# Kernel optimization log

Measured on AMD Instinct MI355X. Metric: run time of the kernel, lower is better.

Reference implementation:

```python
import jax, jax.numpy as jnp
import numpy as np

# Graph geometry: G complete graphs (molecules) of n nodes each.
N_PER_G, G, DEG = 64, 256, 16
H, D = 8, 8
IN_DIM = H * D      # 64
EDGE_DIM = 64
N = N_PER_G * G                      # 16384 nodes
EF = G * N_PER_G * N_PER_G           # 1,048,576 full edges
ES = G * N_PER_G * DEG               # 262,144 sparse edges
SCALE = float(np.sqrt(D))


def _edges():
    n = N_PER_G
    # full graph: all (i -> j) pairs per block, edge id = b*n*n + i*n + j
    ij = np.arange(n * n)
    i, j = ij // n, ij % n
    b = np.arange(G)[:, None]
    src_full = (b * n + i[None, :]).reshape(-1).astype(np.int32)
    dst_full = (b * n + j[None, :]).reshape(-1).astype(np.int32)
    # sparse graph: each dst j receives from DEG distinct sources (j+1..j+DEG mod n)
    jj = np.arange(n)[:, None]
    kk = np.arange(DEG)[None, :]
    ii = (jj + 1 + kk) % n
    eid_block = (ii * n + jj).reshape(-1)                 # [n*DEG]
    sparse_eid = (np.arange(G)[:, None] * n * n + eid_block[None, :]).reshape(-1).astype(np.int32)
    return jnp.asarray(src_full), jnp.asarray(dst_full), jnp.asarray(sparse_eid)


def setup_inputs() -> dict:
    key = jax.random.key(0)
    ks = jax.random.split(key, 16)
    w = lambda k, shape, s=0.05: s * jax.random.normal(k, shape, jnp.float32)
    src_full, dst_full, sparse_eid = _edges()
    return dict(
        h=jax.random.normal(ks[0], (N, IN_DIM), jnp.float32),
        e=jax.random.normal(ks[1], (ES, EDGE_DIM), jnp.float32),
        adj2=jax.random.uniform(ks[2], (EF,), jnp.float32),
        rel_pos_3d=jax.random.normal(ks[3], (EF, H), jnp.float32),
        Wq=w(ks[4], (H * D, IN_DIM)), bq=jnp.zeros((H * D,), jnp.float32),
        Wk=w(ks[5], (H * D, IN_DIM)), bk=jnp.zeros((H * D,), jnp.float32),
        Wv=w(ks[6], (H * D, IN_DIM)), bv=jnp.zeros((H * D,), jnp.float32),
        Wpe=w(ks[7], (H, EDGE_DIM)), bpe=jnp.zeros((H,), jnp.float32),
        Wap=w(ks[8], (EDGE_DIM, H)), bap=jnp.zeros((EDGE_DIM,), jnp.float32),
        Wo=w(ks[9], (H * D, H * D)), bo=jnp.zeros((H * D,), jnp.float32),
        Woe=w(ks[10], (EDGE_DIM, EDGE_DIM)), boe=jnp.zeros((EDGE_DIM,), jnp.float32),
        src_full=src_full, dst_full=dst_full, sparse_eid=sparse_eid,
    )


def reference(h, e, adj2, rel_pos_3d, Wq, bq, Wk, bk, Wv, bv, Wpe, bpe,
              Wap, bap, Wo, bo, Woe, boe, src_full, dst_full, sparse_eid):
    Qh = (h @ Wq.T + bq).reshape(N, H, D)
    Kh = (h @ Wk.T + bk).reshape(N, H, D)
    Vh = (h @ Wv.T + bv).reshape(N, H, D)
    proj_e = e @ Wpe.T + bpe                                   # [ES, H]
    # edge-wise QK dot (src=K, dst=Q), scaled, then gaussian-decay + rel-pos bias
    score = jnp.sum(Kh[src_full] * Qh[dst_full], axis=-1) / SCALE   # [EF, H]
    score = score * adj2[:, None] + rel_pos_3d                      # [EF, H]
    # gather sparse-subgraph scores, project for edge output, add proj_e bias
    sc_sp = score[sparse_eid]                                        # [ES, H]
    e_out_raw = sc_sp @ Wap.T + bap                                  # [ES, EDGE_DIM]
    score = score.at[sparse_eid].set(sc_sp + proj_e)
    # edge softmax over incoming edges of each destination node
    logits = jnp.clip(score, -5.0, 5.0)
    m = jax.ops.segment_max(logits, dst_full, num_segments=N)
    ex = jnp.exp(logits - m[dst_full])
    den = jax.ops.segment_sum(ex, dst_full, num_segments=N)
    attn = ex / den[dst_full]                                        # [EF, H]
    # weighted scatter-sum of source values
    wV = jax.ops.segment_sum(Vh[src_full] * attn[..., None], dst_full, num_segments=N)
    h_out = wV.reshape(N, H * D) @ Wo.T + bo
    e_out = (e_out_raw + e) @ Woe.T + boe
    return h_out, e_out
```

## Files before the change

kernel.cpp:

```cpp
#include <hip/hip_runtime.h>


__global__ __launch_bounds__(512, 2) void qkvpe_kernel(
    const float* __restrict__ h,
    const float* __restrict__ e,
    const float* __restrict__ Wq, const float* __restrict__ bq,
    const float* __restrict__ Wk, const float* __restrict__ bk,
    const float* __restrict__ Wv, const float* __restrict__ bv,
    const float* __restrict__ Wpe, const float* __restrict__ bpe,
    float* __restrict__ Qs, float* __restrict__ Ks, float* __restrict__ Vs,
    float* __restrict__ PEs)
{
    const int t = threadIdx.x;
    if (blockIdx.x < 256) {
        const int b    = blockIdx.x;
        const int lane = t & 63;
        const int wu   = __builtin_amdgcn_readfirstlane(t >> 6);
        const float* hrow = h + (size_t)(b * 64 + lane) * 64;
        float accQ[8], accK[8], accV[8];
        #pragma unroll
        for (int cc = 0; cc < 8; ++cc) {
            const int c = wu * 8 + cc;
            accQ[cc] = bq[c]; accK[cc] = bk[c]; accV[cc] = bv[c];
        }
        #pragma unroll 1
        for (int k0 = 0; k0 < 4; ++k0) {
            float hv[16];
            #pragma unroll
            for (int u = 0; u < 4; ++u) {
                const float4 x = ((const float4*)hrow)[k0 * 4 + u];
                hv[u*4+0] = x.x; hv[u*4+1] = x.y; hv[u*4+2] = x.z; hv[u*4+3] = x.w;
            }
            #pragma unroll
            for (int cc = 0; cc < 8; ++cc) {
                const int c = wu * 8 + cc;
                const float* wq  = Wq + c * 64 + k0 * 16;
                const float* wk  = Wk + c * 64 + k0 * 16;
                const float* wvp = Wv + c * 64 + k0 * 16;
                #pragma unroll
                for (int k = 0; k < 16; ++k) {
                    accQ[cc] = fmaf(hv[k], wq[k],  accQ[cc]);
                    accK[cc] = fmaf(hv[k], wk[k],  accK[cc]);
                    accV[cc] = fmaf(hv[k], wvp[k], accV[cc]);
                }
            }
        }
        const size_t o = (size_t)(b * 64 + lane) * 64 + wu * 8;
        *(float4*)(Qs + o)     = make_float4(accQ[0], accQ[1], accQ[2], accQ[3]);
        *(float4*)(Qs + o + 4) = make_float4(accQ[4], accQ[5], accQ[6], accQ[7]);
        *(float4*)(Ks + o)     = make_float4(accK[0], accK[1], accK[2], accK[3]);
        *(float4*)(Ks + o + 4) = make_float4(accK[4], accK[5], accK[6], accK[7]);
        *(float4*)(Vs + o)     = make_float4(accV[0], accV[1], accV[2], accV[3]);
        *(float4*)(Vs + o + 4) = make_float4(accV[4], accV[5], accV[6], accV[7]);
    } else {
        const int row = (blockIdx.x - 256) * 512 + t;
        const float* erow = e + (size_t)row * 64;
        float acc[8];
        #pragma unroll
        for (int h2 = 0; h2 < 8; ++h2) acc[h2] = bpe[h2];
        #pragma unroll 1
        for (int k0 = 0; k0 < 4; ++k0) {
            float ev[16];
            #pragma unroll
            for (int u = 0; u < 4; ++u) {
                const float4 x = ((const float4*)erow)[k0 * 4 + u];
                ev[u*4+0] = x.x; ev[u*4+1] = x.y; ev[u*4+2] = x.z; ev[u*4+3] = x.w;
            }
            #pragma unroll
            for (int h2 = 0; h2 < 8; ++h2) {
                const float* wp = Wpe + h2 * 64 + k0 * 16;
                #pragma unroll
                for (int k = 0; k < 16; ++k)
                    acc[h2] = fmaf(ev[k], wp[k], acc[h2]);
            }
        }
        float* p0 = PEs + (size_t)row * 8;
        *(float4*)(p0)     = make_float4(acc[0], acc[1], acc[2], acc[3]);
        *(float4*)(p0 + 4) = make_float4(acc[4], acc[5], acc[6], acc[7]);
    }
}

__global__ __launch_bounds__(256, 2) void attn_kernel(
    const float* __restrict__ Qs, const float* __restrict__ Ks,
    const float* __restrict__ Vs, const float* __restrict__ PEs,
    const float* __restrict__ adj2,
    const float* __restrict__ rel,
    float* __restrict__ wVg,
    float* __restrict__ scsp)
{
    const int b2   = blockIdx.x;
    const int b    = b2 >> 1;
    const int joff = (b2 & 1) << 5;
    const int t    = threadIdx.x;
    const int j    = joff + (t >> 3);
    const int hh   = t & 7;

    const float* kB   = Ks + (size_t)b * 4096 + hh * 8;
    const float* vB   = Vs + (size_t)b * 4096 + hh * 8;
    const float* relP = rel + ((size_t)b * 4096 + j) * 8 + hh;
    const float* adjP = adj2 + (size_t)b * 4096 + j;
    const float* peP  = PEs + ((size_t)b * 1024 + j * 16) * 8 + hh;

    float q[8];
    {
        const float* qp = Qs + (size_t)(b * 64 + j) * 64 + hh * 8;
        const float4 a = *(const float4*)qp;
        const float4 c = *(const float4*)(qp + 4);
        q[0]=a.x; q[1]=a.y; q[2]=a.z; q[3]=a.w;
        q[4]=c.x; q[5]=c.y; q[6]=c.z; q[7]=c.w;
    }

    float den = 0.f;
    float wv[8] = {0.f,0.f,0.f,0.f,0.f,0.f,0.f,0.f};
    float sc[16];
    const float inv_scale = 0.35355339059327379f;

    #pragma unroll
    for (int m = 0; m < 16; ++m) {
        const int i = (j + 1 + m) & 63;
        const float4 kA = *(const float4*)(kB + i * 64);
        const float4 kBv = *(const float4*)(kB + i * 64 + 4);
        const float rp = relP[(size_t)i * 512];
        const float a2 = adjP[(size_t)i * 64];
        const float pe = peP[m * 8];
        float s = kA.x * q[0];
        s = fmaf(kA.y, q[1], s); s = fmaf(kA.z, q[2], s); s = fmaf(kA.w, q[3], s);
        s = fmaf(kBv.x, q[4], s); s = fmaf(kBv.y, q[5], s); s = fmaf(kBv.z, q[6], s);
        s = fmaf(kBv.w, q[7], s);
        s = fmaf(s * inv_scale, a2, rp);
        sc[m] = s;
        s += pe;
        s = fminf(fmaxf(s, -5.f), 5.f);
        const float ex = __expf(s);
        den += ex;
        const float4 vA = *(const float4*)(vB + i * 64);
        const float4 vBv = *(const float4*)(vB + i * 64 + 4);
        wv[0] = fmaf(ex, vA.x, wv[0]); wv[1] = fmaf(ex, vA.y, wv[1]);
        wv[2] = fmaf(ex, vA.z, wv[2]); wv[3] = fmaf(ex, vA.w, wv[3]);
        wv[4] = fmaf(ex, vBv.x, wv[4]); wv[5] = fmaf(ex, vBv.y, wv[5]);
        wv[6] = fmaf(ex, vBv.z, wv[6]); wv[7] = fmaf(ex, vBv.w, wv[7]);
    }
    #pragma unroll 8
    for (int m = 16; m < 64; ++m) {
        const int i = (j + 1 + m) & 63;
        const float4 kA = *(const float4*)(kB + i * 64);
        const float4 kBv = *(const float4*)(kB + i * 64 + 4);
        const float rp = relP[(size_t)i * 512];
        const float a2 = adjP[(size_t)i * 64];
        float s = kA.x * q[0];
        s = fmaf(kA.y, q[1], s); s = fmaf(kA.z, q[2], s); s = fmaf(kA.w, q[3], s);
        s = fmaf(kBv.x, q[4], s); s = fmaf(kBv.y, q[5], s); s = fmaf(kBv.z, q[6], s);
        s = fmaf(kBv.w, q[7], s);
        s = fmaf(s * inv_scale, a2, rp);
        s = fminf(fmaxf(s, -5.f), 5.f);
        const float ex = __expf(s);
        den += ex;
        const float4 vA = *(const float4*)(vB + i * 64);
        const float4 vBv = *(const float4*)(vB + i * 64 + 4);
        wv[0] = fmaf(ex, vA.x, wv[0]); wv[1] = fmaf(ex, vA.y, wv[1]);
        wv[2] = fmaf(ex, vA.z, wv[2]); wv[3] = fmaf(ex, vA.w, wv[3]);
        wv[4] = fmaf(ex, vBv.x, wv[4]); wv[5] = fmaf(ex, vBv.y, wv[5]);
        wv[6] = fmaf(ex, vBv.z, wv[6]); wv[7] = fmaf(ex, vBv.w, wv[7]);
    }

    float* sp = scsp + ((size_t)b * 1024 + j * 16) * 8 + hh;
    #pragma unroll
    for (int m = 0; m < 16; ++m) sp[m * 8] = sc[m];

    const float id = 1.f / den;
    float* wp = wVg + (size_t)(b * 64 + j) * 64 + hh * 8;
    *(float4*)(wp)     = make_float4(wv[0]*id, wv[1]*id, wv[2]*id, wv[3]*id);
    *(float4*)(wp + 4) = make_float4(wv[4]*id, wv[5]*id, wv[6]*id, wv[7]*id);
}

__global__ __launch_bounds__(256, 2) void hout_kernel(
    const float* __restrict__ wVg,
    const float* __restrict__ Wo, const float* __restrict__ bo,
    float* __restrict__ h_out)
{
    __shared__ float shWT[64 * 69];
    __shared__ float shWoT[64 * 65];

    const int t    = threadIdx.x;
    const int base = blockIdx.x * 64;

    {
        const int r0 = t >> 2, qq = t & 3;
        const float* ep = wVg + (size_t)(base + r0) * 64 + qq * 16;
        #pragma unroll
        for (int v = 0; v < 4; ++v) {
            const float4 x = ((const float4*)ep)[v];
            const int c = qq * 16 + v * 4;
            shWT[(c + 0) * 69 + r0] = x.x;
            shWT[(c + 1) * 69 + r0] = x.y;
            shWT[(c + 2) * 69 + r0] = x.z;
            shWT[(c + 3) * 69 + r0] = x.w;
        }
    }
    {
        const int c0 = t >> 2, qq = t & 3;
        const float* wp = Wo + c0 * 64 + qq * 16;
        #pragma unroll
        for (int v = 0; v < 4; ++v) {
            const float4 x = ((const float4*)wp)[v];
            const int k = qq * 16 + v * 4;
            shWoT[(k + 0) * 65 + c0] = x.x;
            shWoT[(k + 1) * 65 + c0] = x.y;
            shWoT[(k + 2) * 65 + c0] = x.z;
            shWoT[(k + 3) * 65 + c0] = x.w;
        }
    }
    __syncthreads();

    const int rq = t >> 4;
    const int cq = t & 15;
    float acc[16];
    {
        const float4 bv = *(const float4*)(bo + cq * 4);
        #pragma unroll
        for (int ri = 0; ri < 4; ++ri) {
            acc[ri*4+0] = bv.x; acc[ri*4+1] = bv.y;
            acc[ri*4+2] = bv.z; acc[ri*4+3] = bv.w;
        }
    }
    #pragma unroll
    for (int k = 0; k < 64; ++k) {
        const float4 ev = *(const float4*)&shWT[k * 69 + rq * 4];
        const float4 wk = *(const float4*)&shWoT[k * 65 + cq * 4];
        acc[0]  = fmaf(ev.x, wk.x, acc[0]);  acc[1]  = fmaf(ev.x, wk.y, acc[1]);
        acc[2]  = fmaf(ev.x, wk.z, acc[2]);  acc[3]  = fmaf(ev.x, wk.w, acc[3]);
        acc[4]  = fmaf(ev.y, wk.x, acc[4]);  acc[5]  = fmaf(ev.y, wk.y, acc[5]);
        acc[6]  = fmaf(ev.y, wk.z, acc[6]);  acc[7]  = fmaf(ev.y, wk.w, acc[7]);
        acc[8]  = fmaf(ev.z, wk.x, acc[8]);  acc[9]  = fmaf(ev.z, wk.y, acc[9]);
        acc[10] = fmaf(ev.z, wk.z, acc[10]); acc[11] = fmaf(ev.z, wk.w, acc[11]);
        acc[12] = fmaf(ev.w, wk.x, acc[12]); acc[13] = fmaf(ev.w, wk.y, acc[13]);
        acc[14] = fmaf(ev.w, wk.z, acc[14]); acc[15] = fmaf(ev.w, wk.w, acc[15]);
    }
    #pragma unroll
    for (int ri = 0; ri < 4; ++ri) {
        float* orow = h_out + (size_t)(base + rq * 4 + ri) * 64 + cq * 4;
        *(float4*)orow = make_float4(acc[ri*4+0], acc[ri*4+1], acc[ri*4+2], acc[ri*4+3]);
    }
}

__global__ void prep_kernel(const float* __restrict__ Wap, const float* __restrict__ bap,
                            const float* __restrict__ Woe, const float* __restrict__ boe,
                            float* __restrict__ M2, float* __restrict__ Tm, int hasT)
{
    const int tg = blockIdx.x * 64 + threadIdx.x;
    if (tg < 512) {
        const int c = tg >> 3, hq = tg & 7;
        float s = 0.f;
        #pragma unroll 8
        for (int k = 0; k < 64; ++k) s = fmaf(Woe[c * 64 + k], Wap[k * 8 + hq], s);
        M2[tg] = s;
    } else if (tg < 576) {
        const int c = tg - 512;
        float s = boe[c];
        #pragma unroll 8
        for (int k = 0; k < 64; ++k) s = fmaf(bap[k], Woe[c * 64 + k], s);
        M2[512 + c] = s;
    } else if (hasT && tg < 576 + 73 * 64) {
        const int idx = tg - 576;
        const int k = idx >> 6, c = idx & 63;
        float v;
        if (k < 64) {
            v = Woe[c * 64 + k];
        } else if (k < 72) {
            const int hq = k - 64;
            v = 0.f;
            #pragma unroll 8
            for (int kk = 0; kk < 64; ++kk)
                v = fmaf(Woe[c * 64 + kk], Wap[kk * 8 + hq], v);
        } else {
            v = boe[c];
            #pragma unroll 8
            for (int kk = 0; kk < 64; ++kk)
                v = fmaf(bap[kk], Woe[c * 64 + kk], v);
        }
        Tm[k * 64 + c] = v;
    }
}

__global__ __launch_bounds__(256, 2) void eoutT_kernel(
    const float* __restrict__ e,
    const float* __restrict__ scsp,
    const float* __restrict__ Tm,
    float* __restrict__ e_out)
{
    __shared__ float shET[72 * 69];
    __shared__ float shTm[73 * 64];

    const int t    = threadIdx.x;
    const int base = blockIdx.x * 64;

    {
        const int r0 = t >> 2, qq = t & 3;
        const float* ep = e + (size_t)(base + r0) * 64 + qq * 16;
        #pragma unroll
        for (int v = 0; v < 4; ++v) {
            const float4 x = ((const float4*)ep)[v];
            const int c = qq * 16 + v * 4;
            shET[(c + 0) * 69 + r0] = x.x;
            shET[(c + 1) * 69 + r0] = x.y;
            shET[(c + 2) * 69 + r0] = x.z;
            shET[(c + 3) * 69 + r0] = x.w;
        }
    }
    if (t < 128) {
        const int r = t >> 1, pp = t & 1;
        const float4 s4 = *(const float4*)(scsp + (size_t)(base + r) * 8 + pp * 4);
        shET[(64 + pp * 4 + 0) * 69 + r] = s4.x;
        shET[(64 + pp * 4 + 1) * 69 + r] = s4.y;
        shET[(64 + pp * 4 + 2) * 69 + r] = s4.z;
        shET[(64 + pp * 4 + 3) * 69 + r] = s4.w;
    }
    #pragma unroll
    for (int v = 0; v < 5; ++v) {
        const int fi = v * 256 + t;
        if (fi < 1168)
            *(float4*)&shTm[fi * 4] = *(const float4*)(Tm + fi * 4);
    }
    __syncthreads();

    const int rq = t >> 4;
    const int cq = t & 15;
    float acc[16];
    {
        const float4 bcv = *(const float4*)&shTm[72 * 64 + cq * 4];
        #pragma unroll
        for (int ri = 0; ri < 4; ++ri) {
            acc[ri*4+0] = bcv.x; acc[ri*4+1] = bcv.y;
            acc[ri*4+2] = bcv.z; acc[ri*4+3] = bcv.w;
        }
    }
    #pragma unroll
    for (int k = 0; k < 72; ++k) {
        const float4 ev = *(const float4*)&shET[k * 69 + rq * 4];
        const float4 wk = *(const float4*)&shTm[k * 64 + cq * 4];
        acc[0]  = fmaf(ev.x, wk.x, acc[0]);  acc[1]  = fmaf(ev.x, wk.y, acc[1]);
        acc[2]  = fmaf(ev.x, wk.z, acc[2]);  acc[3]  = fmaf(ev.x, wk.w, acc[3]);
        acc[4]  = fmaf(ev.y, wk.x, acc[4]);  acc[5]  = fmaf(ev.y, wk.y, acc[5]);
        acc[6]  = fmaf(ev.y, wk.z, acc[6]);  acc[7]  = fmaf(ev.y, wk.w, acc[7]);
        acc[8]  = fmaf(ev.z, wk.x, acc[8]);  acc[9]  = fmaf(ev.z, wk.y, acc[9]);
        acc[10] = fmaf(ev.z, wk.z, acc[10]); acc[11] = fmaf(ev.z, wk.w, acc[11]);
        acc[12] = fmaf(ev.w, wk.x, acc[12]); acc[13] = fmaf(ev.w, wk.y, acc[13]);
        acc[14] = fmaf(ev.w, wk.z, acc[14]); acc[15] = fmaf(ev.w, wk.w, acc[15]);
    }
    #pragma unroll
    for (int ri = 0; ri < 4; ++ri) {
        float* orow = e_out + (size_t)(base + rq * 4 + ri) * 64 + cq * 4;
        *(float4*)orow = make_float4(acc[ri*4+0], acc[ri*4+1], acc[ri*4+2], acc[ri*4+3]);
    }
}

__global__ __launch_bounds__(256, 2) void eout_kernel(
    const float* __restrict__ e,
    const float* __restrict__ scsp,
    const float* __restrict__ Woe,
    const float* __restrict__ M2g,
    float* __restrict__ e_out)
{
    __shared__ float shE[64 * 64];
    __shared__ float shS[64 * 8];
    const int t    = threadIdx.x;
    const int base = blockIdx.x * 64;
    {
        const int r = t >> 2, qq = t & 3;
        const float* ep = e + (size_t)(base + r) * 64 + qq * 16;
        #pragma unroll
        for (int u = 0; u < 4; ++u) {
            const float4 x = ((const float4*)ep)[u];
            const int cc = qq * 4 + u;
            *(float4*)&shE[r * 64 + ((cc ^ (r & 15)) << 2)] = x;
        }
    }
    if (t < 128) {
        const int r = t >> 1, pp = t & 1;
        *(float4*)&shS[r * 8 + pp * 4] =
            *(const float4*)(scsp + (size_t)(base + r) * 8 + pp * 4);
    }
    __syncthreads();
    const int w = __builtin_amdgcn_readfirstlane(t >> 6);
    const int r = t & 63;
    float sc[8];
    {
        const float4 a  = *(const float4*)&shS[r * 8];
        const float4 c4 = *(const float4*)&shS[r * 8 + 4];
        sc[0]=a.x; sc[1]=a.y; sc[2]=a.z; sc[3]=a.w;
        sc[4]=c4.x; sc[5]=c4.y; sc[6]=c4.z; sc[7]=c4.w;
    }
    float acc[16];
    #pragma unroll
    for (int u = 0; u < 16; ++u) {
        const int c = w * 16 + u;
        float s = M2g[512 + c];
        #pragma unroll
        for (int hq = 0; hq < 8; ++hq)
            s = fmaf(sc[hq], M2g[c * 8 + hq], s);
        acc[u] = s;
    }
    #pragma unroll
    for (int k0 = 0; k0 < 4; ++k0) {
        float ev[16];
        #pragma unroll
        for (int v = 0; v < 4; ++v) {
            const int cc = k0 * 4 + v;
            const float4 x = *(const float4*)&shE[r * 64 + ((cc ^ (r & 15)) << 2)];
            ev[v*4+0] = x.x; ev[v*4+1] = x.y; ev[v*4+2] = x.z; ev[v*4+3] = x.w;
        }
        #pragma unroll
        for (int u = 0; u < 16; ++u) {
            const float* wr = Woe + (w * 16 + u) * 64 + k0 * 16;
            #pragma unroll
            for (int k = 0; k < 16; ++k)
                acc[u] = fmaf(ev[k], wr[k], acc[u]);
        }
    }
    float* orow = e_out + (size_t)(base + r) * 64 + w * 16;
    #pragma unroll
    for (int u = 0; u < 4; ++u)
        *(float4*)&orow[u * 4] =
            make_float4(acc[u*4+0], acc[u*4+1], acc[u*4+2], acc[u*4+3]);
}

extern "C" void kernel_launch(void* const* d_in, const int* in_sizes, int n_in,
                              void* d_out, int out_size, void* d_ws, size_t ws_size,
                              hipStream_t stream) {
    const float* h    = (const float*)d_in[0];
    const float* e    = (const float*)d_in[1];
    const float* adj2 = (const float*)d_in[2];
    const float* rel  = (const float*)d_in[3];
    const float* Wq   = (const float*)d_in[4];  const float* bq  = (const float*)d_in[5];
    const float* Wk   = (const float*)d_in[6];  const float* bk  = (const float*)d_in[7];
    const float* Wv   = (const float*)d_in[8];  const float* bv  = (const float*)d_in[9];
    const float* Wpe  = (const float*)d_in[10]; const float* bpe = (const float*)d_in[11];
    const float* Wap  = (const float*)d_in[12]; const float* bap = (const float*)d_in[13];
    const float* Wo   = (const float*)d_in[14]; const float* bo  = (const float*)d_in[15];
    const float* Woe  = (const float*)d_in[16]; const float* boe = (const float*)d_in[17];

    float* out  = (float*)d_out;
    float* hout = out;
    float* eout = out + 16384 * 64;
    float* Qs   = eout;
    float* Ks   = eout + 1048576;
    float* Vs   = eout + 2097152;
    float* PEs  = eout + 3145728;
    float* ws   = (float*)d_ws;
    float* scsp = ws;
    float* M2g  = ws + 2097152;
    float* Tm   = ws + 2098176;
    const int hasT = (ws_size >= (size_t)(2098176 + 73 * 64) * sizeof(float)) ? 1 : 0;

    prep_kernel<<<dim3(82), dim3(64), 0, stream>>>(Wap, bap, Woe, boe, M2g, Tm, hasT);
    qkvpe_kernel<<<dim3(768), dim3(512), 0, stream>>>(
        h, e, Wq, bq, Wk, bk, Wv, bv, Wpe, bpe, Qs, Ks, Vs, PEs);
    attn_kernel<<<dim3(512), dim3(256), 0, stream>>>(
        Qs, Ks, Vs, PEs, adj2, rel, hout , scsp);
    hout_kernel<<<dim3(256), dim3(256), 0, stream>>>(hout, Wo, bo, hout);
    if (hasT)
        eoutT_kernel<<<dim3(4096), dim3(256), 0, stream>>>(e, scsp, Tm, eout);
    else
        eout_kernel<<<dim3(4096), dim3(256), 0, stream>>>(e, scsp, Woe, M2g, eout);
}
```

Measured before the change: 130.8 us.

## Pre-transpose adj2/rel in prep kernel and stage K/V/PE in LDS for attention

Adds extra blocks to the QKV/PE kernel that transpose adj2 and rel_pos_3d per graph into a layout contiguous per destination node. The attention kernel then loads those rows with float4 into registers and stages K, V and PE for the whole graph in shared memory, using one 512-thread block per graph. Sparse-edge scores are written in place into the shared PE buffer and copied out in one coalesced pass. This replaces strided global reads with contiguous ones, but it adds an extra full read and write of rel and adj2 through global scratch, uses large register arrays (R and A, 64 each), and drops attention occupancy to one block per CU.

```diff
diff --git a/kernel.cpp b/kernel.cpp
--- a/kernel.cpp
+++ b/kernel.cpp
@@ -4,13 +4,17 @@
 __global__ __launch_bounds__(512, 2) void qkvpe_kernel(
     const float* __restrict__ h,
     const float* __restrict__ e,
+    const float* __restrict__ adj2,
+    const float* __restrict__ rel,
     const float* __restrict__ Wq, const float* __restrict__ bq,
     const float* __restrict__ Wk, const float* __restrict__ bk,
     const float* __restrict__ Wv, const float* __restrict__ bv,
     const float* __restrict__ Wpe, const float* __restrict__ bpe,
     float* __restrict__ Qs, float* __restrict__ Ks, float* __restrict__ Vs,
-    float* __restrict__ PEs)
+    float* __restrict__ PEs, float* __restrict__ relT, float* __restrict__ adjT)
 {
+    __shared__ float shA[64 * 65];
+    __shared__ float shR[8 * 576];
     const int t = threadIdx.x;
     if (blockIdx.x < 256) {
         const int b    = blockIdx.x;
@@ -52,7 +56,7 @@
         *(float4*)(Ks + o + 4) = make_float4(accK[4], accK[5], accK[6], accK[7]);
         *(float4*)(Vs + o)     = make_float4(accV[0], accV[1], accV[2], accV[3]);
         *(float4*)(Vs + o + 4) = make_float4(accV[4], accV[5], accV[6], accV[7]);
-    } else {
+    } else if (blockIdx.x < 768) {
         const int row = (blockIdx.x - 256) * 512 + t;
         const float* erow = e + (size_t)row * 64;
         float acc[8];
@@ -77,96 +81,135 @@
         float* p0 = PEs + (size_t)row * 8;
         *(float4*)(p0)     = make_float4(acc[0], acc[1], acc[2], acc[3]);
         *(float4*)(p0 + 4) = make_float4(acc[4], acc[5], acc[6], acc[7]);
-    }
-}
-
-__global__ __launch_bounds__(256, 2) void attn_kernel(
+    } else {
+        const int b = blockIdx.x - 768;
+        {
+            const float* ap = adj2 + (size_t)b * 4096 + t * 8;
+            #pragma unroll
+            for (int d = 0; d < 8; ++d)
+                shA[((t & 7) * 8 + d) * 65 + (t >> 3)] = ap[d];
+        }
+        __syncthreads();
+        {
+            const int jj = t >> 3, io = (t & 7) * 8;
+            float* op = adjT + (size_t)b * 4096 + jj * 64 + io;
+            #pragma unroll
+            for (int d = 0; d < 8; ++d)
+                op[d] = shA[jj * 65 + io + d];
+        }
+        #pragma unroll 1
+        for (int c = 0; c < 8; ++c) {
+            __syncthreads();
+            {
+                const float* rp = rel + (size_t)b * 32768 + c * 4096 + t * 8;
+                const int i8 = t >> 6;
+                const int g  = t & 63;
+                #pragma unroll
+                for (int d = 0; d < 8; ++d)
+                    shR[i8 * 576 + g * 9 + d] = rp[d];
+            }
+            __syncthreads();
+            {
+                float* op = relT + (size_t)b * 32768 + (size_t)t * 64 + c * 8;
+                const int g = t >> 3, d0 = t & 7;
+                #pragma unroll
+                for (int i8 = 0; i8 < 8; ++i8)
+                    op[i8] = shR[i8 * 576 + g * 9 + d0];
+            }
+        }
+    }
+}
+
+__global__ __launch_bounds__(512, 1) void attn_kernel(
     const float* __restrict__ Qs, const float* __restrict__ Ks,
     const float* __restrict__ Vs, const float* __restrict__ PEs,
-    const float* __restrict__ adj2,
-    const float* __restrict__ rel,
+    const float* __restrict__ adjT,
+    const float* __restrict__ relT,
     float* __restrict__ wVg,
     float* __restrict__ scsp)
 {
-    const int b2   = blockIdx.x;
-    const int b    = b2 >> 1;
-    const int joff = (b2 & 1) << 5;
-    const int t    = threadIdx.x;
-    const int j    = joff + (t >> 3);
-    const int hh   = t & 7;
-
-    const float* kB   = Ks + (size_t)b * 4096 + hh * 8;
-    const float* vB   = Vs + (size_t)b * 4096 + hh * 8;
-    const float* relP = rel + ((size_t)b * 4096 + j) * 8 + hh;
-    const float* adjP = adj2 + (size_t)b * 4096 + j;
-    const float* peP  = PEs + ((size_t)b * 1024 + j * 16) * 8 + hh;
-
+    __shared__ float shK[64 * 64];
+    __shared__ float shV[64 * 64];
+    __shared__ float shPE[1024 * 8];
+
+    const int b  = blockIdx.x;
+    const int t  = threadIdx.x;
+    const int j  = t >> 3;
+    const int hh = t & 7;
+
+    const float* rT = relT + (size_t)b * 32768 + (size_t)t * 64;
+    const float* aT = adjT + (size_t)b * 4096 + (size_t)j * 64;
+    float R[64], A[64];
+    #pragma unroll
+    for (int u = 0; u < 16; ++u) {
+        const float4 x = *(const float4*)(rT + u * 4);
+        R[u*4+0] = x.x; R[u*4+1] = x.y; R[u*4+2] = x.z; R[u*4+3] = x.w;
+        const float4 y = *(const float4*)(aT + u * 4);
+        A[u*4+0] = y.x; A[u*4+1] = y.y; A[u*4+2] = y.z; A[u*4+3] = y.w;
+    }
+    {
+        const float4* srcK = (const float4*)(Ks + (size_t)b * 4096);
+        const float4* srcV = (const float4*)(Vs + (size_t)b * 4096);
+        float4* dK = (float4*)shK; float4* dV = (float4*)shV;
+        #pragma unroll
+        for (int u = 0; u < 2; ++u) {
+            dK[u * 512 + t] = srcK[u * 512 + t];
+            dV[u * 512 + t] = srcV[u * 512 + t];
+        }
+        const float4* srcP = (const float4*)(PEs + (size_t)b * 8192);
+        float4* dP = (float4*)shPE;
+        #pragma unroll
+        for (int u = 0; u < 4; ++u)
+            dP[u * 512 + t] = srcP[u * 512 + t];
+    }
     float q[8];
     {
         const float* qp = Qs + (size_t)(b * 64 + j) * 64 + hh * 8;
         const float4 a = *(const float4*)qp;
-        const float4 c = *(const float4*)(qp + 4);
+        const float4 c4 = *(const float4*)(qp + 4);
         q[0]=a.x; q[1]=a.y; q[2]=a.z; q[3]=a.w;
-        q[4]=c.x; q[5]=c.y; q[6]=c.z; q[7]=c.w;
-    }
+        q[4]=c4.x; q[5]=c4.y; q[6]=c4.z; q[7]=c4.w;
+    }
+    __syncthreads();
 
     float den = 0.f;
     float wv[8] = {0.f,0.f,0.f,0.f,0.f,0.f,0.f,0.f};
-    float sc[16];
     const float inv_scale = 0.35355339059327379f;
-
-    #pragma unroll
-    for (int m = 0; m < 16; ++m) {
-        const int i = (j + 1 + m) & 63;
-        const float4 kA = *(const float4*)(kB + i * 64);
-        const float4 kBv = *(const float4*)(kB + i * 64 + 4);
-        const float rp = relP[(size_t)i * 512];
-        const float a2 = adjP[(size_t)i * 64];
-        const float pe = peP[m * 8];
+    #pragma unroll
+    for (int i = 0; i < 64; ++i) {
+        const float4 kA = *(const float4*)&shK[i * 64 + hh * 8];
+        const float4 kC = *(const float4*)&shK[i * 64 + hh * 8 + 4];
         float s = kA.x * q[0];
         s = fmaf(kA.y, q[1], s); s = fmaf(kA.z, q[2], s); s = fmaf(kA.w, q[3], s);
-        s = fmaf(kBv.x, q[4], s); s = fmaf(kBv.y, q[5], s); s = fmaf(kBv.z, q[6], s);
-        s = fmaf(kBv.w, q[7], s);
-        s = fmaf(s * inv_scale, a2, rp);
-        sc[m] = s;
-        s += pe;
+        s = fmaf(kC.x, q[4], s); s = fmaf(kC.y, q[5], s); s = fmaf(kC.z, q[6], s);
+        s = fmaf(kC.w, q[7], s);
+        s = fmaf(s * inv_scale, A[i], R[i]);
+        const int kidx = (i - j - 1) & 63;
+        if (kidx < 16) {
+            const int x = (j * 16 + kidx) * 8 + hh;
+            const float pe = shPE[x];
+            shPE[x] = s;
+            s += pe;
+        }
         s = fminf(fmaxf(s, -5.f), 5.f);
         const float ex = __expf(s);
         den += ex;
-        const float4 vA = *(const float4*)(vB + i * 64);
-        const float4 vBv = *(const float4*)(vB + i * 64 + 4);
+        const float4 vA = *(const float4*)&shV[i * 64 + hh * 8];
+        const float4 vC = *(const float4*)&shV[i * 64 + hh * 8 + 4];
         wv[0] = fmaf(ex, vA.x, wv[0]); wv[1] = fmaf(ex, vA.y, wv[1]);
         wv[2] = fmaf(ex, vA.z, wv[2]); wv[3] = fmaf(ex, vA.w, wv[3]);
-        wv[4] = fmaf(ex, vBv.x, wv[4]); wv[5] = fmaf(ex, vBv.y, wv[5]);
-        wv[6] = fmaf(ex, vBv.z, wv[6]); wv[7] = fmaf(ex, vBv.w, wv[7]);
-    }
-    #pragma unroll 8
-    for (int m = 16; m < 64; ++m) {
-        const int i = (j + 1 + m) & 63;
-        const float4 kA = *(const float4*)(kB + i * 64);
-        const float4 kBv = *(const float4*)(kB + i * 64 + 4);
-        const float rp = relP[(size_t)i * 512];
-        const float a2 = adjP[(size_t)i * 64];
-        float s = kA.x * q[0];
-        s = fmaf(kA.y, q[1], s); s = fmaf(kA.z, q[2], s); s = fmaf(kA.w, q[3], s);
-        s = fmaf(kBv.x, q[4], s); s = fmaf(kBv.y, q[5], s); s = fmaf(kBv.z, q[6], s);
-        s = fmaf(kBv.w, q[7], s);
-        s = fmaf(s * inv_scale, a2, rp);
-        s = fminf(fmaxf(s, -5.f), 5.f);
-        const float ex = __expf(s);
-        den += ex;
-        const float4 vA = *(const float4*)(vB + i * 64);
-        const float4 vBv = *(const float4*)(vB + i * 64 + 4);
-        wv[0] = fmaf(ex, vA.x, wv[0]); wv[1] = fmaf(ex, vA.y, wv[1]);
-        wv[2] = fmaf(ex, vA.z, wv[2]); wv[3] = fmaf(ex, vA.w, wv[3]);
-        wv[4] = fmaf(ex, vBv.x, wv[4]); wv[5] = fmaf(ex, vBv.y, wv[5]);
-        wv[6] = fmaf(ex, vBv.z, wv[6]); wv[7] = fmaf(ex, vBv.w, wv[7]);
-    }
-
-    float* sp = scsp + ((size_t)b * 1024 + j * 16) * 8 + hh;
-    #pragma unroll
-    for (int m = 0; m < 16; ++m) sp[m * 8] = sc[m];
-
+        wv[4] = fmaf(ex, vC.x, wv[4]); wv[5] = fmaf(ex, vC.y, wv[5]);
+        wv[6] = fmaf(ex, vC.z, wv[6]); wv[7] = fmaf(ex, vC.w, wv[7]);
+    }
+    __syncthreads();
+
+    {
+        const float4* src = (const float4*)shPE;
+        float4* dst = (float4*)(scsp + (size_t)b * 8192);
+        #pragma unroll
+        for (int u = 0; u < 4; ++u)
+            dst[u * 512 + t] = src[u * 512 + t];
+    }
     const float id = 1.f / den;
     float* wp = wVg + (size_t)(b * 64 + j) * 64 + hh * 8;
     *(float4*)(wp)     = make_float4(wv[0]*id, wv[1]*id, wv[2]*id, wv[3]*id);
@@ -446,6 +489,8 @@
     float* Ks   = eout + 1048576;
     float* Vs   = eout + 2097152;
     float* PEs  = eout + 3145728;
+    float* relT = eout + 5242880;
+    float* adjT = eout + 13631488;
     float* ws   = (float*)d_ws;
     float* scsp = ws;
     float* M2g  = ws + 2097152;
@@ -453,10 +498,11 @@
     const int hasT = (ws_size >= (size_t)(2098176 + 73 * 64) * sizeof(float)) ? 1 : 0;
 
     prep_kernel<<<dim3(82), dim3(64), 0, stream>>>(Wap, bap, Woe, boe, M2g, Tm, hasT);
-    qkvpe_kernel<<<dim3(768), dim3(512), 0, stream>>>(
-        h, e, Wq, bq, Wk, bk, Wv, bv, Wpe, bpe, Qs, Ks, Vs, PEs);
-    attn_kernel<<<dim3(512), dim3(256), 0, stream>>>(
-        Qs, Ks, Vs, PEs, adj2, rel, hout , scsp);
+    qkvpe_kernel<<<dim3(1024), dim3(512), 0, stream>>>(
+        h, e, adj2, rel, Wq, bq, Wk, bk, Wv, bv, Wpe, bpe,
+        Qs, Ks, Vs, PEs, relT, adjT);
+    attn_kernel<<<dim3(256), dim3(512), 0, stream>>>(
+        Qs, Ks, Vs, PEs, adjT, relT, hout , scsp);
     hout_kernel<<<dim3(256), dim3(256), 0, stream>>>(hout, Wo, bo, hout);
     if (hasT)
         eoutT_kernel<<<dim3(4096), dim3(256), 0, stream>>>(e, scsp, Tm, eout);
```

New measurement: 223.2 us. 70.7% more time.
